# Kernel optimization log

Measured on AMD Instinct MI355X. Metric: run time of the kernel, lower is better.

The kernel has to match this reference:

```python
import jax, jax.numpy as jnp
import numpy as np

ALPHA = 1.0
BETA = 0.05


def setup_inputs() -> dict:
    key = jax.random.key(0)
    kQ, kK, kV, kH, kDQ, kDK = jax.random.split(key, 6)
    N, M, D, d = 8192, 8192, 128, 128
    Q = jax.random.normal(kQ, (N, D), dtype=jnp.float32)
    K = jax.random.normal(kK, (M, D), dtype=jnp.float32)
    V = jax.random.normal(kV, (M, d), dtype=jnp.float32)
    # Doob h-potential must be strictly positive (it is logged)
    h = jax.random.uniform(kH, (N,), dtype=jnp.float32, minval=0.5, maxval=1.5)
    log_d_q = 0.1 * jax.random.normal(kDQ, (N,), dtype=jnp.float32)
    log_d_k = 0.1 * jax.random.normal(kDK, (M,), dtype=jnp.float32)
    return {"Q": Q, "K": K, "V": V, "h": h, "log_d_q": log_d_q, "log_d_k": log_d_k}


def reference(Q, K, V, h, log_d_q, log_d_k):
    # s_ij = -beta*||q_i - k_j||^2 - alpha*(log_d_q[i] + log_d_k[j]) + log h_i - log h_j
    q_norm2 = jnp.sum(Q * Q, axis=-1)  # (N,)
    k_norm2 = jnp.sum(K * K, axis=-1)  # (M,)
    log_h = jnp.log(h)                  # (N,) ; Q and K share h (self-attention points)
    qk = jnp.einsum("nd,md->nm", Q, K)  # (N, M)
    s = BETA * (2.0 * qk - q_norm2[:, None] - k_norm2[None, :])
    s = s - ALPHA * (log_d_q[:, None] + log_d_k[None, :])
    s = s + log_h[:, None] - log_h[None, :]
    # row-softmax = Markov normalisation; lse = log row sums of un-normalised kernel
    lse = jax.nn.logsumexp(s, axis=-1)          # (N,)
    P = jnp.exp(s - lse[:, None])               # (N, M)
    out = jnp.einsum("nm,md->nd", P, V)          # (N, d)
    return out, lse
```

## Files before the change

### kernel.cpp

```cpp
#include <hip/hip_runtime.h>
#include <cstddef>
#include <cstdint>

#define BETA 0.05f

typedef unsigned short u16;
typedef unsigned int u32;
typedef __attribute__((ext_vector_type(8))) short bf16x8;
typedef __attribute__((ext_vector_type(16))) float f32x16;
typedef __attribute__((ext_vector_type(4))) u32 u32x4;

constexpr int NQ = 8192;
constexpr int NK = 8192;
constexpr int DH = 128;
constexpr int SPLITS = 8;
constexpr int CHUNK = NK / SPLITS;
constexpr int KVB = 64;
constexpr int STEPS = CHUNK / KVB;
constexpr int KSTEP = 16384;
constexpr int VSTEP = 16384;
constexpr int LDS_BYTES = 2 * KSTEP + 2 * VSTEP + 4096;


__device__ __forceinline__ u16 f2bf(float x) {
  union { float f; u32 u; } v; v.f = x;
  u32 r = (v.u + 0x7fffu + ((v.u >> 16) & 1u)) >> 16;
  return (u16)r;
}
__device__ __forceinline__ float fexp2(float x) {
#if __has_builtin(__builtin_amdgcn_exp2f)
  return __builtin_amdgcn_exp2f(x);
#else
  return exp2f(x);
#endif
}
__device__ __forceinline__ void gload_lds16(const void* gsrc, void* ldst) {
  __builtin_amdgcn_global_load_lds(
      (const __attribute__((address_space(1))) u32*)gsrc,
      (__attribute__((address_space(3))) u32*)ldst, 16, 0, 0);
}

__global__ void prep_all(const float* __restrict__ Q, const float* __restrict__ ldq,
                         const float* __restrict__ K, const float* __restrict__ ldk,
                         const float* __restrict__ h, const float* __restrict__ V,
                         u16* __restrict__ Qa, u16* __restrict__ Kf,
                         float* __restrict__ B2f, float* __restrict__ arow,
                         u16* __restrict__ Vf) {
  __shared__ float tile[64][65];
  const int bi = blockIdx.x;
  const int lane = threadIdx.x & 63;
  if (bi < NQ / 4) {
    const int row = bi * 4 + (threadIdx.x >> 6);
    const float2 q2 = *(const float2*)(Q + (size_t)row * DH + lane * 2);
    float sq = q2.x * q2.x + q2.y * q2.y;
#pragma unroll
    for (int off = 32; off > 0; off >>= 1) sq += __shfl_xor(sq, off);
    const float SC = 2.0f * BETA * 1.4426950408889634f;
    ushort2 o; o.x = f2bf(SC * q2.x); o.y = f2bf(SC * q2.y);
    *(ushort2*)(Qa + (size_t)row * DH + lane * 2) = o;
    if (lane == 0) arow[row] = -BETA * sq - ldq[row] + logf(h[row]);
  } else if (bi < NQ / 2) {
    const int row = (bi - NQ / 4) * 4 + (threadIdx.x >> 6);
    const float2 k2 = *(const float2*)(K + (size_t)row * DH + lane * 2);
    float sq = k2.x * k2.x + k2.y * k2.y;
#pragma unroll
    for (int off = 32; off > 0; off >>= 1) sq += __shfl_xor(sq, off);
    ushort2 o; o.x = f2bf(k2.x); o.y = f2bf(k2.y);
    char* dst = (char*)Kf + ((size_t)(row >> 5) * 8 + (lane >> 3)) * 1024
              + ((((lane >> 2) & 1) * 32) + (row & 31)) * 16 + (lane & 3) * 4;
    *(ushort2*)dst = o;
    if (lane == 0) {
      const float b2 = (-BETA * sq - ldk[row] - logf(h[row])) * 1.4426950408889634f;
      const int w = row & 31;
      B2f[(size_t)(row >> 5) * 32 + ((w >> 2) & 1) * 16 + (w & 3) + 4 * (w >> 3)] = b2;
    }
  } else {
    const int vb = bi - NQ / 2;
    const int j0 = (vb >> 1) * 64;
    const int d0 = (vb & 1) * 64;
    const int t = threadIdx.x;
    const int r = t >> 4;
    const int c = (t & 15) * 4;
#pragma unroll
    for (int rr = r; rr < 64; rr += 16) {
      const float4 v = *(const float4*)(V + (size_t)(j0 + rr) * DH + d0 + c);
      tile[rr][c + 0] = v.x; tile[rr][c + 1] = v.y;
      tile[rr][c + 2] = v.z; tile[rr][c + 3] = v.w;
    }
    __syncthreads();
    const int kv8i = t & 7;
    const int dl0 = t >> 3;
#pragma unroll
    for (int dd = dl0; dd < 64; dd += 32) {
      const int dg = d0 + dd;
      const int b16g = (j0 >> 4) + (kv8i >> 1);
      const int hi = kv8i & 1;
      union { u32x4 q; u16 s[8]; } pk;
#pragma unroll
      for (int m = 0; m < 8; ++m) pk.s[m] = f2bf(tile[kv8i * 8 + m][dd]);
      *(u32x4*)((char*)Vf + ((size_t)(b16g * 4 + (dg >> 5)) * 1024)
                + ((hi * 32) + (dg & 31)) * 16) = pk.q;
    }
  }
}

__device__ __forceinline__ void smpv2(const f32x16& sA, const f32x16& sB,
                                      const char* vbh,
                                      f32x16 acc[4], float& lsum, int hi) {
  float p[16];
#pragma unroll
  for (int r = 0; r < 16; ++r) p[r] = fexp2(sA[r] + sB[r]);
  {
    float t0 = (p[0] + p[1]) + (p[2] + p[3]);
    float t1 = (p[4] + p[5]) + (p[6] + p[7]);
    float t2 = (p[8] + p[9]) + (p[10] + p[11]);
    float t3 = (p[12] + p[13]) + (p[14] + p[15]);
    lsum += (t0 + t1) + (t2 + t3);
  }
  u32 pk0, pk1, pk2, pk3, pk4, pk5, pk6, pk7;
  asm("v_cvt_pk_bf16_f32 %0, %1, %2" : "=v"(pk0) : "v"(p[0]),  "v"(p[1]));
  asm("v_cvt_pk_bf16_f32 %0, %1, %2" : "=v"(pk1) : "v"(p[2]),  "v"(p[3]));
  asm("v_cvt_pk_bf16_f32 %0, %1, %2" : "=v"(pk2) : "v"(p[4]),  "v"(p[5]));
  asm("v_cvt_pk_bf16_f32 %0, %1, %2" : "=v"(pk3) : "v"(p[6]),  "v"(p[7]));
  asm("v_cvt_pk_bf16_f32 %0, %1, %2" : "=v"(pk4) : "v"(p[8]),  "v"(p[9]));
  asm("v_cvt_pk_bf16_f32 %0, %1, %2" : "=v"(pk5) : "v"(p[10]), "v"(p[11]));
  asm("v_cvt_pk_bf16_f32 %0, %1, %2" : "=v"(pk6) : "v"(p[12]), "v"(p[13]));
  asm("v_cvt_pk_bf16_f32 %0, %1, %2" : "=v"(pk7) : "v"(p[14]), "v"(p[15]));
  const bool hb = (hi != 0);
#pragma unroll
  for (int ksl = 0; ksl < 2; ++ksl) {
    const u32 a0 = ksl ? pk4 : pk0, a1 = ksl ? pk5 : pk1;
    const u32 b0 = ksl ? pk6 : pk2, b1 = ksl ? pk7 : pk3;
    const u32 own0 = hb ? b0 : a0, own1 = hb ? b1 : a1;
    const u32 snd0 = hb ? a0 : b0, snd1 = hb ? a1 : b1;
    const u32 rcv0 = (u32)__shfl_xor((int)snd0, 32);
    const u32 rcv1 = (u32)__shfl_xor((int)snd1, 32);
    union { u32x4 u; bf16x8 b; } pa;
    pa.u[0] = hb ? rcv0 : own0;
    pa.u[1] = hb ? rcv1 : own1;
    pa.u[2] = hb ? own0 : rcv0;
    pa.u[3] = hb ? own1 : rcv1;
#pragma unroll
    for (int dt = 0; dt < 4; ++dt) {
      const bf16x8 vf = *(const bf16x8*)(vbh + (ksl * 4 + dt) * 1024);
      acc[dt] = __builtin_amdgcn_mfma_f32_32x32x16_bf16(pa.b, vf, acc[dt], 0, 0, 0);
    }
  }
}

__global__ __launch_bounds__(512) void attn_main(
    const u16* __restrict__ Qa, const u16* __restrict__ Kf,
    const u16* __restrict__ Vf, const float* __restrict__ B2f,
    u16* __restrict__ Opart, float* __restrict__ Lpart) {
  extern __shared__ __align__(16) char lds[];
  char* ldsK = lds;
  char* ldsV = lds + 2 * KSTEP;
  char* ldsB = lds + 2 * KSTEP + 2 * VSTEP;

  const int tid = threadIdx.x;
  const int wid = tid >> 6;
  const int lane = tid & 63;
  const int hi = lane >> 5;
  const int ln31 = lane & 31;
  const int bi = blockIdx.x;
  const int ks = bi & 7;
  const int qg = bi >> 3;
  const int kvbase = ks * CHUNK;
  const int qrow0 = qg * 256 + wid * 32;

  bf16x8 qf[8];
#pragma unroll
  for (int sl = 0; sl < 8; ++sl)
    qf[sl] = *(const bf16x8*)((const char*)Qa + (size_t)(qrow0 + ln31) * 256 + sl * 32 + hi * 16);

  f32x16 acc[4];
#pragma unroll
  for (int dt = 0; dt < 4; ++dt)
#pragma unroll
    for (int r = 0; r < 16; ++r) acc[dt][r] = 0.0f;
  float lsum = 0.0f;

  const char* KfG = (const char*)Kf + ((size_t)(kvbase >> 5) * 8) * 1024 + lane * 16;
  const char* VfG = (const char*)Vf + ((size_t)(kvbase >> 4) * 4) * 1024 + lane * 16;

  auto STAGE = [&](int buf, int step) {
    const char* ksrc = KfG + (size_t)step * KSTEP + wid * 2048;
    const char* vsrc = VfG + (size_t)step * VSTEP + wid * 2048;
    char* kdst = ldsK + buf * KSTEP + wid * 2048;
    char* vdst = ldsV + buf * VSTEP + wid * 2048;
    gload_lds16(ksrc, kdst);
    gload_lds16(ksrc + 1024, kdst + 1024);
    gload_lds16(vsrc, vdst);
    gload_lds16(vsrc + 1024, vdst + 1024);
  };

  if (wid < 4)
    gload_lds16((const char*)B2f + (size_t)(kvbase >> 5) * 128 + wid * 1024 + lane * 16,
                ldsB + wid * 1024);
  STAGE(0, 0);
  __syncthreads();

  for (int t = 0; t < STEPS; ++t) {
    const int cur = t & 1;
    if (t < STEPS - 1) STAGE(cur ^ 1, t + 1);

    const char* kb = ldsK + cur * KSTEP + lane * 16;
    const char* vb = ldsV + cur * VSTEP + lane * 16;

    f32x16 sA0 = *(const f32x16*)(ldsB + t * 256 + hi * 64);
    f32x16 sB0;
#pragma unroll
    for (int r = 0; r < 16; ++r) sB0[r] = 0.0f;
#pragma unroll
    for (int sl = 0; sl < 8; ++sl) {
      const bf16x8 kf = *(const bf16x8*)(kb + sl * 1024);
      if (sl & 1)
        sB0 = __builtin_amdgcn_mfma_f32_32x32x16_bf16(kf, qf[sl], sB0, 0, 0, 0);
      else
        sA0 = __builtin_amdgcn_mfma_f32_32x32x16_bf16(kf, qf[sl], sA0, 0, 0, 0);
    }
    smpv2(sA0, sB0, vb, acc, lsum, hi);

    f32x16 sA1 = *(const f32x16*)(ldsB + t * 256 + 128 + hi * 64);
    f32x16 sB1;
#pragma unroll
    for (int r = 0; r < 16; ++r) sB1[r] = 0.0f;
#pragma unroll
    for (int sl = 0; sl < 8; ++sl) {
      const bf16x8 kf = *(const bf16x8*)(kb + (8 + sl) * 1024);
      if (sl & 1)
        sB1 = __builtin_amdgcn_mfma_f32_32x32x16_bf16(kf, qf[sl], sB1, 0, 0, 0);
      else
        sA1 = __builtin_amdgcn_mfma_f32_32x32x16_bf16(kf, qf[sl], sA1, 0, 0, 0);
    }
    smpv2(sA1, sB1, vb + 8192, acc, lsum, hi);

    __syncthreads();
  }

  lsum += __shfl_xor(lsum, 32);
  u16* op = Opart + ((size_t)ks * NQ + qrow0) * DH;
#pragma unroll
  for (int dt = 0; dt < 4; ++dt)
#pragma unroll
    for (int r = 0; r < 16; ++r) {
      const int q = (r & 3) + 8 * (r >> 2) + 4 * hi;
      op[(size_t)q * DH + dt * 32 + ln31] = f2bf(acc[dt][r]);
    }
  if (hi == 0) Lpart[(size_t)ks * NQ + qrow0 + ln31] = lsum;
}

__global__ void combine(const u16* __restrict__ Opart, const float* __restrict__ Lpart,
                        const float* __restrict__ arow, float* __restrict__ out,
                        float* __restrict__ lse) {
  const int idx = blockIdx.x * 256 + threadIdx.x;
  const int row = idx >> 5;
  const int d4 = (idx & 31) * 4;
  float o0 = 0.f, o1 = 0.f, o2 = 0.f, o3 = 0.f;
  float L = 0.f;
#pragma unroll
  for (int s = 0; s < SPLITS; ++s) {
    const ushort4 v = *(const ushort4*)(Opart + ((size_t)s * NQ + row) * DH + d4);
    union { u32 u; float f; } c0, c1, c2, c3;
    c0.u = ((u32)v.x) << 16; c1.u = ((u32)v.y) << 16;
    c2.u = ((u32)v.z) << 16; c3.u = ((u32)v.w) << 16;
    o0 += c0.f; o1 += c1.f; o2 += c2.f; o3 += c3.f;
    L += Lpart[(size_t)s * NQ + row];
  }
  const float inv = 1.0f / L;
  *(float4*)(out + (size_t)row * DH + d4) =
      make_float4(o0 * inv, o1 * inv, o2 * inv, o3 * inv);
  if ((idx & 31) == 0) lse[row] = logf(L) + arow[row];
}

extern "C" void kernel_launch(void* const* d_in, const int* in_sizes, int n_in,
                              void* d_out, int out_size, void* d_ws, size_t ws_size,
                              hipStream_t stream) {
  const float* Q = (const float*)d_in[0];
  const float* K = (const float*)d_in[1];
  const float* V = (const float*)d_in[2];
  const float* h = (const float*)d_in[3];
  const float* ldq = (const float*)d_in[4];
  const float* ldk = (const float*)d_in[5];

  char* ws = (char*)d_ws;
  u16* Qa    = (u16*)(ws + 0);
  u16* Kf    = (u16*)(ws + 2097152);
  u16* Vf    = (u16*)(ws + 4194304);
  float* B2f   = (float*)(ws + 6291456);
  float* arow  = (float*)(ws + 6324224);
  u16* Opart = (u16*)(ws + 6356992);
  float* Lpart = (float*)(ws + 23134208);

  float* out = (float*)d_out;
  float* lse = out + (size_t)NQ * DH;

  hipFuncSetAttribute(reinterpret_cast<const void*>(attn_main),
                      hipFuncAttributeMaxDynamicSharedMemorySize, LDS_BYTES);

  prep_all<<<NQ / 2 + 256, 256, 0, stream>>>(Q, ldq, K, ldk, h, V, Qa, Kf, B2f, arow, Vf);
  attn_main<<<(NQ / 256) * SPLITS, 512, LDS_BYTES, stream>>>(Qa, Kf, Vf, B2f, Opart, Lpart);
  combine<<<NQ * 32 / 256, 256, 0, stream>>>(Opart, Lpart, arow, out, lse);
}
```

Measured before the change: 57.48 us.

## Process two query tiles per wave to reuse K/V fragments and double KV splits

Each wave now computes attention for 64 query rows as two 32-row tiles. Each K and V fragment read from LDS feeds MFMAs for both tiles, halving LDS read traffic per query row and giving two independent MFMA chains. To keep the grid at the same block count, the KV dimension is split 16 ways instead of 8, and launch bounds request two blocks per CU. The trade-offs are higher register pressure, with a risk of spills, and twice as many partial outputs for the combine kernel to read.

```diff
diff --git a/kernel.cpp b/kernel.cpp
--- a/kernel.cpp
+++ b/kernel.cpp
@@ -13,13 +13,13 @@
 constexpr int NQ = 8192;
 constexpr int NK = 8192;
 constexpr int DH = 128;
-constexpr int SPLITS = 8;
+constexpr int SPLITS = 16;
 constexpr int CHUNK = NK / SPLITS;
 constexpr int KVB = 64;
 constexpr int STEPS = CHUNK / KVB;
 constexpr int KSTEP = 16384;
 constexpr int VSTEP = 16384;
-constexpr int LDS_BYTES = 2 * KSTEP + 2 * VSTEP + 4096;
+constexpr int LDS_BYTES = 2 * KSTEP + 2 * VSTEP + 2048;
 
 
 __device__ __forceinline__ u16 f2bf(float x) {
@@ -104,12 +104,11 @@
   }
 }
 
-__device__ __forceinline__ void smpv2(const f32x16& sA, const f32x16& sB,
-                                      const char* vbh,
-                                      f32x16 acc[4], float& lsum, int hi) {
+__device__ __forceinline__ void mkpa(const f32x16& s, int hi, float& lsum,
+                                     bf16x8* pa ) {
   float p[16];
 #pragma unroll
-  for (int r = 0; r < 16; ++r) p[r] = fexp2(sA[r] + sB[r]);
+  for (int r = 0; r < 16; ++r) p[r] = fexp2(s[r]);
   {
     float t0 = (p[0] + p[1]) + (p[2] + p[3]);
     float t1 = (p[4] + p[5]) + (p[6] + p[7]);
@@ -135,20 +134,16 @@
     const u32 snd0 = hb ? a0 : b0, snd1 = hb ? a1 : b1;
     const u32 rcv0 = (u32)__shfl_xor((int)snd0, 32);
     const u32 rcv1 = (u32)__shfl_xor((int)snd1, 32);
-    union { u32x4 u; bf16x8 b; } pa;
-    pa.u[0] = hb ? rcv0 : own0;
-    pa.u[1] = hb ? rcv1 : own1;
-    pa.u[2] = hb ? own0 : rcv0;
-    pa.u[3] = hb ? own1 : rcv1;
-#pragma unroll
-    for (int dt = 0; dt < 4; ++dt) {
-      const bf16x8 vf = *(const bf16x8*)(vbh + (ksl * 4 + dt) * 1024);
-      acc[dt] = __builtin_amdgcn_mfma_f32_32x32x16_bf16(pa.b, vf, acc[dt], 0, 0, 0);
-    }
-  }
-}
-
-__global__ __launch_bounds__(512) void attn_main(
+    union { u32x4 u; bf16x8 b; } pw;
+    pw.u[0] = hb ? rcv0 : own0;
+    pw.u[1] = hb ? rcv1 : own1;
+    pw.u[2] = hb ? own0 : rcv0;
+    pw.u[3] = hb ? own1 : rcv1;
+    pa[ksl] = pw.b;
+  }
+}
+
+__global__ __launch_bounds__(512, 2) void attn_main(
     const u16* __restrict__ Qa, const u16* __restrict__ Kf,
     const u16* __restrict__ Vf, const float* __restrict__ B2f,
     u16* __restrict__ Opart, float* __restrict__ Lpart) {
@@ -163,22 +158,24 @@
   const int hi = lane >> 5;
   const int ln31 = lane & 31;
   const int bi = blockIdx.x;
-  const int ks = bi & 7;
-  const int qg = bi >> 3;
+  const int ks = bi & 15;
+  const int qg = bi >> 4;
   const int kvbase = ks * CHUNK;
-  const int qrow0 = qg * 256 + wid * 32;
-
-  bf16x8 qf[8];
-#pragma unroll
-  for (int sl = 0; sl < 8; ++sl)
-    qf[sl] = *(const bf16x8*)((const char*)Qa + (size_t)(qrow0 + ln31) * 256 + sl * 32 + hi * 16);
-
-  f32x16 acc[4];
+  const int qrow0 = qg * 512 + wid * 64;
+
+  bf16x8 qfa[8], qfb[8];
+#pragma unroll
+  for (int sl = 0; sl < 8; ++sl) {
+    qfa[sl] = *(const bf16x8*)((const char*)Qa + (size_t)(qrow0 + ln31) * 256 + sl * 32 + hi * 16);
+    qfb[sl] = *(const bf16x8*)((const char*)Qa + (size_t)(qrow0 + 32 + ln31) * 256 + sl * 32 + hi * 16);
+  }
+
+  f32x16 accA[4], accB[4];
 #pragma unroll
   for (int dt = 0; dt < 4; ++dt)
 #pragma unroll
-    for (int r = 0; r < 16; ++r) acc[dt][r] = 0.0f;
-  float lsum = 0.0f;
+    for (int r = 0; r < 16; ++r) { accA[dt][r] = 0.0f; accB[dt][r] = 0.0f; }
+  float lsumA = 0.0f, lsumB = 0.0f;
 
   const char* KfG = (const char*)Kf + ((size_t)(kvbase >> 5) * 8) * 1024 + lane * 16;
   const char* VfG = (const char*)Vf + ((size_t)(kvbase >> 4) * 4) * 1024 + lane * 16;
@@ -194,7 +191,7 @@
     gload_lds16(vsrc + 1024, vdst + 1024);
   };
 
-  if (wid < 4)
+  if (wid < 2)
     gload_lds16((const char*)B2f + (size_t)(kvbase >> 5) * 128 + wid * 1024 + lane * 16,
                 ldsB + wid * 1024);
   STAGE(0, 0);
@@ -207,47 +204,51 @@
     const char* kb = ldsK + cur * KSTEP + lane * 16;
     const char* vb = ldsV + cur * VSTEP + lane * 16;
 
-    f32x16 sA0 = *(const f32x16*)(ldsB + t * 256 + hi * 64);
-    f32x16 sB0;
-#pragma unroll
-    for (int r = 0; r < 16; ++r) sB0[r] = 0.0f;
-#pragma unroll
-    for (int sl = 0; sl < 8; ++sl) {
-      const bf16x8 kf = *(const bf16x8*)(kb + sl * 1024);
-      if (sl & 1)
-        sB0 = __builtin_amdgcn_mfma_f32_32x32x16_bf16(kf, qf[sl], sB0, 0, 0, 0);
-      else
-        sA0 = __builtin_amdgcn_mfma_f32_32x32x16_bf16(kf, qf[sl], sA0, 0, 0, 0);
-    }
-    smpv2(sA0, sB0, vb, acc, lsum, hi);
-
-    f32x16 sA1 = *(const f32x16*)(ldsB + t * 256 + 128 + hi * 64);
-    f32x16 sB1;
-#pragma unroll
-    for (int r = 0; r < 16; ++r) sB1[r] = 0.0f;
-#pragma unroll
-    for (int sl = 0; sl < 8; ++sl) {
-      const bf16x8 kf = *(const bf16x8*)(kb + (8 + sl) * 1024);
-      if (sl & 1)
-        sB1 = __builtin_amdgcn_mfma_f32_32x32x16_bf16(kf, qf[sl], sB1, 0, 0, 0);
-      else
-        sA1 = __builtin_amdgcn_mfma_f32_32x32x16_bf16(kf, qf[sl], sA1, 0, 0, 0);
-    }
-    smpv2(sA1, sB1, vb + 8192, acc, lsum, hi);
+#pragma unroll
+    for (int h = 0; h < 2; ++h) {
+      const f32x16 b2v = *(const f32x16*)(ldsB + t * 256 + h * 128 + hi * 64);
+      f32x16 sA = b2v, sB = b2v;
+      const char* kbh = kb + h * 8192;
+#pragma unroll
+      for (int sl = 0; sl < 8; ++sl) {
+        const bf16x8 kf = *(const bf16x8*)(kbh + sl * 1024);
+        sA = __builtin_amdgcn_mfma_f32_32x32x16_bf16(kf, qfa[sl], sA, 0, 0, 0);
+        sB = __builtin_amdgcn_mfma_f32_32x32x16_bf16(kf, qfb[sl], sB, 0, 0, 0);
+      }
+
+      bf16x8 paA[2], paB[2];
+      mkpa(sA, hi, lsumA, paA);
+      mkpa(sB, hi, lsumB, paB);
+
+      const char* vbh = vb + h * 8192;
+#pragma unroll
+      for (int ksl = 0; ksl < 2; ++ksl)
+#pragma unroll
+        for (int dt = 0; dt < 4; ++dt) {
+          const bf16x8 vf = *(const bf16x8*)(vbh + ksl * 4096 + dt * 1024);
+          accA[dt] = __builtin_amdgcn_mfma_f32_32x32x16_bf16(paA[ksl], vf, accA[dt], 0, 0, 0);
+          accB[dt] = __builtin_amdgcn_mfma_f32_32x32x16_bf16(paB[ksl], vf, accB[dt], 0, 0, 0);
+        }
+    }
 
     __syncthreads();
   }
 
-  lsum += __shfl_xor(lsum, 32);
+  lsumA += __shfl_xor(lsumA, 32);
+  lsumB += __shfl_xor(lsumB, 32);
   u16* op = Opart + ((size_t)ks * NQ + qrow0) * DH;
 #pragma unroll
   for (int dt = 0; dt < 4; ++dt)
 #pragma unroll
     for (int r = 0; r < 16; ++r) {
       const int q = (r & 3) + 8 * (r >> 2) + 4 * hi;
-      op[(size_t)q * DH + dt * 32 + ln31] = f2bf(acc[dt][r]);
-    }
-  if (hi == 0) Lpart[(size_t)ks * NQ + qrow0 + ln31] = lsum;
+      op[(size_t)q * DH + dt * 32 + ln31] = f2bf(accA[dt][r]);
+      op[(size_t)(32 + q) * DH + dt * 32 + ln31] = f2bf(accB[dt][r]);
+    }
+  if (hi == 0) {
+    Lpart[(size_t)ks * NQ + qrow0 + ln31] = lsumA;
+    Lpart[(size_t)ks * NQ + qrow0 + 32 + ln31] = lsumB;
+  }
 }
 
 __global__ void combine(const u16* __restrict__ Opart, const float* __restrict__ Lpart,
@@ -290,7 +291,7 @@
   float* B2f   = (float*)(ws + 6291456);
   float* arow  = (float*)(ws + 6324224);
   u16* Opart = (u16*)(ws + 6356992);
-  float* Lpart = (float*)(ws + 23134208);
+  float* Lpart = (float*)(ws + 39911424);
 
   float* out = (float*)d_out;
   float* lse = out + (size_t)NQ * DH;
@@ -299,6 +300,6 @@
                       hipFuncAttributeMaxDynamicSharedMemorySize, LDS_BYTES);
 
   prep_all<<<NQ / 2 + 256, 256, 0, stream>>>(Q, ldq, K, ldk, h, V, Qa, Kf, B2f, arow, Vf);
-  attn_main<<<(NQ / 256) * SPLITS, 512, LDS_BYTES, stream>>>(Qa, Kf, Vf, B2f, Opart, Lpart);
+  attn_main<<<(NQ / 512) * SPLITS, 512, LDS_BYTES, stream>>>(Qa, Kf, Vf, B2f, Opart, Lpart);
   combine<<<NQ * 32 / 256, 256, 0, stream>>>(Opart, Lpart, arow, out, lse);
 }
```

New measurement: 68.72 us. 1.2x slower.
